# Performance work log

Measured on AMD Instinct MI355X. Metric: run time of the kernel, lower is better.

Reference implementation:

```python
import jax, jax.numpy as jnp
import numpy as np

# Arithmetic boolean logic on {0,1} floats (differentiable surrogate used by SNN gates):
#   xor(a,b) = a + b - 2ab
#   full-adder: s = a^b^c ; cout = ab + c*(a^b)   (terms mutually exclusive)

def _full_adder(a, b, c):
    x = a + b - 2.0 * a * b          # a xor b
    s = x + c - 2.0 * x * c          # (a xor b) xor c
    cout = a * b + c * x             # carry out
    return s, cout


def setup_inputs() -> dict:
    key = jax.random.key(0)
    kA, kB = jax.random.split(key)
    N = 8388608  # 2**23 rows
    A = jnp.round(jax.random.uniform(kA, (N, 8), dtype=jnp.float32))
    B = jnp.round(jax.random.uniform(kB, (N, 8), dtype=jnp.float32))
    Cin = jnp.zeros((N, 1), dtype=jnp.float32)
    return {"A": A, "B": B, "Cin": Cin}


def reference(A, B, Cin):
    # A, B: [N, 8] MSB first; ripple from bit 7 (LSB) down to bit 0 (MSB).
    carry = Cin  # [N, 1]
    sums = [None] * 8
    for i in [7, 6, 5, 4, 3, 2, 1, 0]:  # fixed 8-step carry chain
        s, carry = _full_adder(A[..., i:i + 1], B[..., i:i + 1], carry)
        sums[i] = s
    return jnp.concatenate(sums, axis=-1), carry
```

## Files before the change

kernel.cpp:

```cpp
#include <hip/hip_runtime.h>


__global__ __launch_bounds__(256) void Adder8Bit_kernel(
    const float4* __restrict__ A4,
    const float4* __restrict__ B4,
    const float*  __restrict__ Cin,
    float4*       __restrict__ S4,
    float*        __restrict__ Cout,
    int N)
{
    int i = blockIdx.x * blockDim.x + threadIdx.x;
    if (i >= N) return;

    float4 a0 = A4[2 * i];
    float4 a1 = A4[2 * i + 1];
    float4 b0 = B4[2 * i];
    float4 b1 = B4[2 * i + 1];
    float c = Cin[i];

    float a[8] = {a0.x, a0.y, a0.z, a0.w, a1.x, a1.y, a1.z, a1.w};
    float b[8] = {b0.x, b0.y, b0.z, b0.w, b1.x, b1.y, b1.z, b1.w};
    float s[8];

    #pragma unroll
    for (int k = 7; k >= 0; --k) {
        float ab = a[k] * b[k];
        float x  = a[k] + b[k] - 2.0f * ab;
        s[k]     = x + c - 2.0f * x * c;
        c        = ab + c * x;
    }

    S4[2 * i]     = make_float4(s[0], s[1], s[2], s[3]);
    S4[2 * i + 1] = make_float4(s[4], s[5], s[6], s[7]);
    Cout[i] = c;
}

extern "C" void kernel_launch(void* const* d_in, const int* in_sizes, int n_in,
                              void* d_out, int out_size, void* d_ws, size_t ws_size,
                              hipStream_t stream) {
    const float* A   = (const float*)d_in[0];
    const float* B   = (const float*)d_in[1];
    const float* Cin = (const float*)d_in[2];
    float* out = (float*)d_out;

    const int N = in_sizes[0] / 8;

    float4* S4   = (float4*)out;
    float*  Cout = out + (size_t)8 * N;

    const int block = 256;
    const int grid  = (N + block - 1) / block;

    Adder8Bit_kernel<<<grid, block, 0, stream>>>(
        (const float4*)A, (const float4*)B, Cin, S4, Cout, N);
}
```

Measured before the change: 625.0 us.

## Split each row across two threads and use bitwise full-adder on float bits

Each 8-bit row is now handled by two adjacent threads, one per 4-bit half. The high half speculatively computes its carry and passes it to the low half through a lane shuffle. The full adder works on raw float bit patterns with XOR/AND/OR, which holds only because the inputs are exactly 0.0 or 1.0 (1.0f's bits survive AND/OR/XOR). The aim is contiguous uint4 accesses per thread and more threads for this memory-bound kernel. The cost is duplicated adder work and a restriction to exact binary inputs.

```diff
diff --git a/kernel.cpp b/kernel.cpp
--- a/kernel.cpp
+++ b/kernel.cpp
@@ -1,56 +1,69 @@
 #include <hip/hip_runtime.h>
 
 
+__device__ __forceinline__ unsigned fa(unsigned a, unsigned b, unsigned c,
+                                       unsigned& s) {
+    unsigned x = a ^ b;
+    s = x ^ c;
+    return (a & b) | (c & x);
+}
+
 __global__ __launch_bounds__(256) void Adder8Bit_kernel(
-    const float4* __restrict__ A4,
-    const float4* __restrict__ B4,
-    const float*  __restrict__ Cin,
-    float4*       __restrict__ S4,
-    float*        __restrict__ Cout,
-    int N)
+    const uint4* __restrict__ A4,
+    const uint4* __restrict__ B4,
+    const unsigned* __restrict__ Cin,
+    uint4*       __restrict__ S4,
+    unsigned*    __restrict__ Cout,
+    int halves)
 {
-    int i = blockIdx.x * blockDim.x + threadIdx.x;
-    if (i >= N) return;
+    int t = blockIdx.x * blockDim.x + threadIdx.x;
+    if (t >= halves) return;
 
-    float4 a0 = A4[2 * i];
-    float4 a1 = A4[2 * i + 1];
-    float4 b0 = B4[2 * i];
-    float4 b1 = B4[2 * i + 1];
-    float c = Cin[i];
+    int r     = t >> 1;
+    int isLSB = t & 1;
 
-    float a[8] = {a0.x, a0.y, a0.z, a0.w, a1.x, a1.y, a1.z, a1.w};
-    float b[8] = {b0.x, b0.y, b0.z, b0.w, b1.x, b1.y, b1.z, b1.w};
-    float s[8];
+    uint4 a = A4[t];
+    uint4 b = B4[t];
+    unsigned cin0 = Cin[r];
 
-    #pragma unroll
-    for (int k = 7; k >= 0; --k) {
-        float ab = a[k] * b[k];
-        float x  = a[k] + b[k] - 2.0f * ab;
-        s[k]     = x + c - 2.0f * x * c;
-        c        = ab + c * x;
-    }
+    uint4 s1;
+    unsigned c = cin0;
+    c = fa(a.w, b.w, c, s1.w);
+    c = fa(a.z, b.z, c, s1.z);
+    c = fa(a.y, b.y, c, s1.y);
+    c = fa(a.x, b.x, c, s1.x);
 
-    S4[2 * i]     = make_float4(s[0], s[1], s[2], s[3]);
-    S4[2 * i + 1] = make_float4(s[4], s[5], s[6], s[7]);
-    Cout[i] = c;
+    unsigned cprev = (unsigned)__shfl_xor((int)c, 1);
+
+    unsigned cin = isLSB ? cin0 : cprev;
+    uint4 s2;
+    c = cin;
+    c = fa(a.w, b.w, c, s2.w);
+    c = fa(a.z, b.z, c, s2.z);
+    c = fa(a.y, b.y, c, s2.y);
+    c = fa(a.x, b.x, c, s2.x);
+
+    S4[t] = s2;
+    if (!isLSB) Cout[r] = c;
 }
 
 extern "C" void kernel_launch(void* const* d_in, const int* in_sizes, int n_in,
                               void* d_out, int out_size, void* d_ws, size_t ws_size,
                               hipStream_t stream) {
-    const float* A   = (const float*)d_in[0];
-    const float* B   = (const float*)d_in[1];
-    const float* Cin = (const float*)d_in[2];
-    float* out = (float*)d_out;
+    const unsigned* A   = (const unsigned*)d_in[0];
+    const unsigned* B   = (const unsigned*)d_in[1];
+    const unsigned* Cin = (const unsigned*)d_in[2];
+    unsigned* out = (unsigned*)d_out;
 
-    const int N = in_sizes[0] / 8;
+    const int N      = in_sizes[0] / 8;
+    const int halves = 2 * N;
 
-    float4* S4   = (float4*)out;
-    float*  Cout = out + (size_t)8 * N;
+    uint4*    S4   = (uint4*)out;
+    unsigned* Cout = out + (size_t)8 * N;
 
     const int block = 256;
-    const int grid  = (N + block - 1) / block;
+    const int grid  = (halves + block - 1) / block;
 
     Adder8Bit_kernel<<<grid, block, 0, stream>>>(
-        (const float4*)A, (const float4*)B, Cin, S4, Cout, N);
+        (const uint4*)A, (const uint4*)B, Cin, S4, Cout, halves);
 }
```

After: 619.8 us. About the same (-0.8%).
